# Performance work log

Measured on AMD Instinct MI355X. Metric: run time of the kernel, lower is better.

Reference implementation:

```python
import jax, jax.numpy as jnp
import numpy as np

DIM = 512
HEADS = 16
DIM_HEAD = 64
INNER = HEADS * DIM_HEAD
MAX_T = 32
BASE = 10000.0


def rotate_half(t):
    t1, t2 = jnp.split(t, 2, axis=-1)
    return jnp.concatenate((-t2, t1), axis=-1)


def setup_inputs() -> dict:
    key = jax.random.key(0)
    ks = jax.random.split(key, 12)
    B, T, S = 2, 16, 128
    x = jax.random.normal(ks[0], (B, T, S, DIM), dtype=jnp.float32)
    y = jax.random.normal(ks[1], (B, T, S, DIM), dtype=jnp.float32)
    temporal_mask = jax.random.randint(ks[2], (B, T, T), 0, 2).astype(jnp.int32)
    sc = 1.0 / np.sqrt(DIM)
    Wq = jax.random.normal(ks[3], (DIM, INNER), dtype=jnp.float32) * sc
    Wk = jax.random.normal(ks[4], (DIM, INNER), dtype=jnp.float32) * sc
    Wv = jax.random.normal(ks[5], (DIM, INNER), dtype=jnp.float32) * sc
    Wo = jax.random.normal(ks[6], (INNER, DIM), dtype=jnp.float32) / np.sqrt(INNER)
    bo = jnp.zeros((DIM,), dtype=jnp.float32)
    pos_emb = jax.random.normal(ks[7], (MAX_T, DIM), dtype=jnp.float32)
    gate_w = jax.random.normal(ks[8], (DIM, 1), dtype=jnp.float32) * sc
    gate_b = jnp.zeros((1,), dtype=jnp.float32)
    return {"x": x, "y": y, "temporal_mask": temporal_mask, "Wq": Wq, "Wk": Wk,
            "Wv": Wv, "Wo": Wo, "bo": bo, "pos_emb": pos_emb,
            "gate_w": gate_w, "gate_b": gate_b}


def reference(x, y, temporal_mask, Wq, Wk, Wv, Wo, bo, pos_emb, gate_w, gate_b):
    B, T, S, D = x.shape
    n = T * S
    scale = DIM_HEAD ** (-0.5)
    # temporal positional embedding (T <= MAX_T path)
    tp = pos_emb[:T][None, :, None, :]  # [1,T,1,D]
    x = x + tp
    y = y + tp
    xf = x.reshape(B, n, D)
    yf = y.reshape(B, n, D)
    # NOTE: k is computed from x (as in the source), v from y
    q = (xf @ Wq).reshape(B, n, HEADS, DIM_HEAD).transpose(0, 2, 1, 3)
    k = (xf @ Wk).reshape(B, n, HEADS, DIM_HEAD).transpose(0, 2, 1, 3)
    v = (yf @ Wv).reshape(B, n, HEADS, DIM_HEAD).transpose(0, 2, 1, 3)
    # RoPE over flattened token index
    inv_freq = 1.0 / (BASE ** (jnp.arange(0, DIM_HEAD, 2, dtype=jnp.float32) / DIM_HEAD))
    freqs = jnp.arange(n, dtype=jnp.float32)[:, None] * inv_freq[None, :]  # [n, d/2]
    emb = jnp.concatenate((freqs, freqs), axis=-1)  # [n, d]
    fc = jnp.cos(emb)[None, None, :, :]
    fs = jnp.sin(emb)[None, None, :, :]
    q = q * fc + rotate_half(q) * fs
    k = k * fc + rotate_half(k) * fs
    dots = jnp.einsum('bhid,bhjd->bhij', q, k) * scale  # [B,H,n,n]
    # expand temporal mask [B,T,T] -> [B,1,n,n] block structure
    m = jnp.repeat(jnp.repeat(temporal_mask, S, axis=1), S, axis=2)[:, None, :, :]
    dots = jnp.where(m == 0, -jnp.inf, dots)
    attn = jax.nn.softmax(dots, axis=-1)
    out = jnp.einsum('bhij,bhjd->bhid', attn, v)  # [B,H,n,d]
    out = out.transpose(0, 2, 1, 3).reshape(B, n, INNER)
    out = out @ Wo + bo
    out = out.reshape(B, T, S, D)
    gate = jax.nn.sigmoid(out @ gate_w + gate_b)  # [B,T,S,1]
    return out * gate
```

## Files before the change

### kernel.cpp

```cpp
#include <hip/hip_runtime.h>
#include <hip/hip_bf16.h>

typedef __attribute__((ext_vector_type(4))) short short4v;
typedef __attribute__((ext_vector_type(8))) short short8v;
typedef __attribute__((ext_vector_type(4))) float float4v;
typedef __attribute__((ext_vector_type(2))) unsigned int uint2v;
typedef __attribute__((ext_vector_type(4))) unsigned int uint4v;

#define NTOK 2048
#define MROWS 4096
#define DMODEL 512
#define NINNER 1024
#define DH 64
#define HH 16
#define LOG2E 1.4426950408889634f

__device__ __forceinline__ unsigned short b2s(float f) {
    __hip_bfloat16 h = __float2bfloat16(f);
    return __builtin_bit_cast(unsigned short, h);
}
__device__ __forceinline__ float bf2f(unsigned short h) {
    unsigned int u = ((unsigned int)h) << 16;
    return __builtin_bit_cast(float, u);
}

__device__ __forceinline__ float4v mfma32(short8v a, short8v b, float4v c) {
    return __builtin_amdgcn_mfma_f32_16x16x32_bf16(a, b, c, 0, 0, 0);
}

__device__ __forceinline__ void gld16(const void* g, void* l) {
    __builtin_amdgcn_global_load_lds((const __attribute__((address_space(1))) void*)g,
                                     (__attribute__((address_space(3))) void*)l, 16, 0, 0);
}

__global__ void k_pre(const float* __restrict__ x, const float* __restrict__ y,
                      const float* __restrict__ pe,
                      unsigned short* __restrict__ xpb, unsigned short* __restrict__ ypb,
                      const float* __restrict__ Wq, const float* __restrict__ Wk,
                      const float* __restrict__ Wv, const float* __restrict__ Wo,
                      const float* __restrict__ gwv, const float* __restrict__ gbv,
                      const float* __restrict__ bo,
                      unsigned short* __restrict__ wall, unsigned short* __restrict__ wot,
                      float* __restrict__ ctab, float* __restrict__ stab,
                      unsigned short* __restrict__ gvp, float* __restrict__ bgp) {
    __shared__ float tl[64][65];
    const int blk = blockIdx.x;
    const int tid = threadIdx.x;
    if (blk < 2048) {
        int e0 = (blk * 256 + tid) * 4;
        int row = e0 >> 9, col = e0 & 511;
        int t = (row & (NTOK - 1)) >> 7;
        const float4v xv = *(const float4v*)(x + e0);
        const float4v yv = *(const float4v*)(y + e0);
        const float4v pv = *(const float4v*)(pe + t * DMODEL + col);
        short4v xo, yo;
#pragma unroll
        for (int i = 0; i < 4; ++i) {
            xo[i] = (short)b2s(xv[i] + pv[i]);
            yo[i] = (short)b2s(yv[i] + pv[i]);
        }
        *(short4v*)(xpb + e0) = xo;
        *(short4v*)(ypb + e0) = yo;
    } else if (blk < 2560) {
        int t = blk - 2048;
        const float* W;
        unsigned short* dst;
        int K, N, k0, n0;
        if (t < 384) {
            int which = t / 128, tile = t % 128;
            W = (which == 0) ? Wq : (which == 1) ? Wk : Wv;
            dst = wall + (size_t)which * 1024 * 512;
            K = 512; N = 1024;
            k0 = (tile >> 4) * 64; n0 = (tile & 15) * 64;
        } else {
            int tile = t - 384;
            W = Wo; dst = wot;
            K = 1024; N = 512;
            k0 = (tile >> 3) * 64; n0 = (tile & 7) * 64;
        }
        int tx = tid & 63, ty4 = tid >> 6;
#pragma unroll
        for (int p = 0; p < 16; ++p) {
            int ky = p * 4 + ty4;
            tl[ky][tx] = W[(size_t)(k0 + ky) * N + n0 + tx];
        }
        __syncthreads();
#pragma unroll
        for (int p = 0; p < 16; ++p) {
            int ny = p * 4 + ty4;
            dst[(size_t)(n0 + ny) * K + k0 + tx] = b2s(tl[tx][ny]);
        }
    } else if (blk < 2816) {
        int idx = (blk - 2560) * 256 + tid;
        int p = idx >> 5, j = idx & 31;
        float invf = powf(10000.0f, -(float)(2 * j) * (1.0f / 64.0f));
        float f = (float)p * invf;
        ctab[idx] = cosf(f);
        stab[idx] = sinf(f);
    } else if (blk < 2832) {
        int base = (blk - 2816) * 64;
        int w = tid >> 6, l = tid & 63, l16 = l & 15, g = l >> 4;
        int row = base + w * 16 + l16;
        const float* wr = Wo + (size_t)row * 512 + g * 128;
        const float* gr = gwv + g * 128;
        float s = 0.f;
#pragma unroll
        for (int t = 0; t < 32; ++t) {
            float4v a = *(const float4v*)(wr + t * 4);
            float4v b = *(const float4v*)(gr + t * 4);
            s += a[0] * b[0] + a[1] * b[1] + a[2] * b[2] + a[3] * b[3];
        }
        s += __shfl_xor(s, 16);
        s += __shfl_xor(s, 32);
        if (g == 0) gvp[row] = b2s(s);
    } else {
        if (tid < 64) {
            float s = 0.f;
#pragma unroll
            for (int t = 0; t < 8; ++t) s += bo[tid + t * 64] * gwv[tid + t * 64];
#pragma unroll
            for (int off = 32; off > 0; off >>= 1) s += __shfl_xor(s, off);
            if (tid == 0) bgp[0] = s + gbv[0];
        }
    }
}

__global__ __launch_bounds__(256) void k_qkv(const unsigned short* __restrict__ A,
                                             const unsigned short* __restrict__ A2,
                                             const unsigned short* __restrict__ Bt,
                                             unsigned short* __restrict__ Cq,
                                             unsigned short* __restrict__ Ck,
                                             unsigned short* __restrict__ Cvv,
                                             const float* __restrict__ ctab,
                                             const float* __restrict__ stab,
                                             float scale) {
    __shared__ unsigned short Ab[2][4096];
    __shared__ unsigned short Bb[2][4096];
    const int tid = threadIdx.x;
    const int w = tid >> 6, l = tid & 63, l16 = l & 15, g = l >> 4;
    const int wm = w >> 1, wn = w & 1;
    const int m0 = blockIdx.y * 128, n0 = blockIdx.x * 128;
    const unsigned short* Ap = (n0 >= 2048) ? A2 : A;
    float4v acc[4][4];
#pragma unroll
    for (int i = 0; i < 4; ++i)
#pragma unroll
        for (int j = 0; j < 4; ++j) acc[i][j] = (float4v){0.f, 0.f, 0.f, 0.f};

    auto stage = [&](int t, int buf) {
        int k0 = t * 32;
#pragma unroll
        for (int it = 0; it < 2; ++it) {
            int f = it * 4 + w;
            gld16(Ap + (size_t)(m0 + f * 16 + l16) * 512 + k0 + g * 8, &Ab[buf][f * 512]);
            gld16(Bt + (size_t)(n0 + f * 16 + l16) * 512 + k0 + g * 8, &Bb[buf][f * 512]);
        }
    };

    stage(0, 0);
    __syncthreads();
    for (int t = 0; t < 16; ++t) {
        const int cur = t & 1;
        if (t + 1 < 16) stage(t + 1, cur ^ 1);
        short8v af[4], bf[4];
#pragma unroll
        for (int mi = 0; mi < 4; ++mi)
            af[mi] = *(const short8v*)&Ab[cur][(wm * 4 + mi) * 512 + l * 8];
#pragma unroll
        for (int nj = 0; nj < 4; ++nj)
            bf[nj] = *(const short8v*)&Bb[cur][(wn * 4 + nj) * 512 + l * 8];
        __builtin_amdgcn_s_setprio(1);
#pragma unroll
        for (int mi = 0; mi < 4; ++mi)
#pragma unroll
            for (int nj = 0; nj < 4; ++nj)
                acc[mi][nj] = mfma32(af[mi], bf[nj], acc[mi][nj]);
        __builtin_amdgcn_s_setprio(0);
        __syncthreads();
    }

    const int hh = (n0 + wn * 64) >> 6;
    const int head = hh & 15;
    if (hh < 32) {
        unsigned short* out = (hh < 16) ? Cq : Ck;
        const float sc = (hh < 16) ? scale : 1.0f;
#pragma unroll
        for (int mi = 0; mi < 4; ++mi)
#pragma unroll
            for (int r = 0; r < 4; ++r) {
                int row = m0 + wm * 64 + mi * 16 + g * 4 + r;
                int b = row >> 11, pos = row & (NTOK - 1);
                const float* cr = ctab + pos * 32;
                const float* sr = stab + pos * 32;
                unsigned short* ob = out + (size_t)((b * HH + head) * NTOK + pos) * DH;
#pragma unroll
                for (int nj = 0; nj < 2; ++nj) {
                    int j = nj * 16 + l16;
                    float c = cr[j], s = sr[j];
                    float v1 = acc[mi][nj][r], v2 = acc[mi][nj + 2][r];
                    ob[j] = b2s((v1 * c - v2 * s) * sc);
                    ob[j + 32] = b2s((v2 * c + v1 * s) * sc);
                }
            }
    } else {
#pragma unroll
        for (int mi = 0; mi < 4; ++mi)
#pragma unroll
            for (int nj = 0; nj < 4; ++nj) {
                int d = nj * 16 + l16;
                int row0 = m0 + wm * 64 + mi * 16 + g * 4;
                int b = row0 >> 11, pos0 = row0 & (NTOK - 1);
                short4v o;
#pragma unroll
                for (int r = 0; r < 4; ++r) o[r] = (short)b2s(acc[mi][nj][r]);
                *(short4v*)(Cvv + (size_t)((b * HH + head) * DH + d) * NTOK + pos0) = o;
            }
    }
}

__global__ __launch_bounds__(256) void k_gatev(const unsigned short* __restrict__ otm,
                                               const unsigned short* __restrict__ gv,
                                               const float* __restrict__ bgp,
                                               float* __restrict__ glog) {
    int row = blockIdx.x * 4 + (threadIdx.x >> 6);
    int l = threadIdx.x & 63;
    const unsigned short* pr = otm + (size_t)row * NINNER;
    float acc = 0.f;
#pragma unroll
    for (int c = 0; c < 2; ++c) {
        short8v a = *(const short8v*)(pr + (c * 64 + l) * 8);
        short8v b = *(const short8v*)(gv + (c * 64 + l) * 8);
#pragma unroll
        for (int j = 0; j < 8; ++j)
            acc = fmaf(bf2f((unsigned short)a[j]), bf2f((unsigned short)b[j]), acc);
    }
#pragma unroll
    for (int off = 32; off > 0; off >>= 1) acc += __shfl_xor(acc, off);
    if (l == 0) glog[row] = 1.0f / (1.0f + __expf(-(acc + bgp[0])));
}

__global__ __launch_bounds__(256) void k_oproj(const unsigned short* __restrict__ A,
                                               const unsigned short* __restrict__ Bt,
                                               const float* __restrict__ bo,
                                               const float* __restrict__ glog,
                                               float* __restrict__ out) {
    __shared__ unsigned short Ab[2][4096];
    __shared__ unsigned short Bb[2][2048];
    const int tid = threadIdx.x;
    const int w = tid >> 6, l = tid & 63, l16 = l & 15, g = l >> 4;
    const int m0 = blockIdx.y * 128, n0 = blockIdx.x * 64;
    float4v acc[2][4];
#pragma unroll
    for (int i = 0; i < 2; ++i)
#pragma unroll
        for (int j = 0; j < 4; ++j) acc[i][j] = (float4v){0.f, 0.f, 0.f, 0.f};

    auto stage = [&](int t, int buf) {
        int k0 = t * 32;
#pragma unroll
        for (int s = 0; s < 2; ++s) {
            int fi = s * 4 + w;
            gld16(A + (size_t)(m0 + fi * 16 + l16) * 1024 + k0 + g * 8, &Ab[buf][fi * 512]);
        }
        gld16(Bt + (size_t)(n0 + w * 16 + l16) * 1024 + k0 + g * 8, &Bb[buf][w * 512]);
    };

    stage(0, 0);
    __syncthreads();
    for (int t = 0; t < 32; ++t) {
        const int cur = t & 1;
        if (t + 1 < 32) stage(t + 1, cur ^ 1);
        short8v af[2], bf[4];
#pragma unroll
        for (int mi = 0; mi < 2; ++mi)
            af[mi] = *(const short8v*)&Ab[cur][(w * 2 + mi) * 512 + l * 8];
#pragma unroll
        for (int nj = 0; nj < 4; ++nj)
            bf[nj] = *(const short8v*)&Bb[cur][nj * 512 + l * 8];
        __builtin_amdgcn_s_setprio(1);
#pragma unroll
        for (int mi = 0; mi < 2; ++mi)
#pragma unroll
            for (int nj = 0; nj < 4; ++nj)
                acc[mi][nj] = mfma32(af[mi], bf[nj], acc[mi][nj]);
        __builtin_amdgcn_s_setprio(0);
        __syncthreads();
    }
#pragma unroll
    for (int mi = 0; mi < 2; ++mi) {
        float gl[4];
#pragma unroll
        for (int r = 0; r < 4; ++r)
            gl[r] = glog[m0 + w * 32 + mi * 16 + g * 4 + r];
#pragma unroll
        for (int nj = 0; nj < 4; ++nj) {
            int col = n0 + nj * 16 + l16;
            float bv = bo[col];
#pragma unroll
            for (int r = 0; r < 4; ++r) {
                int row = m0 + w * 32 + mi * 16 + g * 4 + r;
                out[(size_t)row * 512 + col] = (acc[mi][nj][r] + bv) * gl[r];
            }
        }
    }
}

__global__ __launch_bounds__(512) void k_attn(const unsigned short* __restrict__ qh,
                                              const unsigned short* __restrict__ kh,
                                              const unsigned short* __restrict__ vt,
                                              const int* __restrict__ tmask,
                                              unsigned short* __restrict__ otmp) {
    __shared__ unsigned short Kb[3][4096];
    __shared__ unsigned short Vb[2][4096];
    __shared__ int tlist[33];
    const int blk = blockIdx.x;
    const int u = (blk & 7) * 64 + (blk >> 3);
    const int ti = u & 15, h = (u >> 4) & 15, b = u >> 8;
    const int tid = threadIdx.x, w = tid >> 6, l = tid & 63, l16 = l & 15, g = l >> 4;
    if (tid == 0) {
        int c = 0;
        for (int j = 0; j < 16; ++j)
            if (tmask[(b * 16 + ti) * 16 + j]) { tlist[c++] = 2 * j; tlist[c++] = 2 * j + 1; }
        tlist[32] = c;
    }
    __syncthreads();
    const int cnt = tlist[32];
    const unsigned short* qb = qh + (size_t)((b * HH + h) * NTOK) * DH;
    const unsigned short* kb = kh + (size_t)((b * HH + h) * NTOK) * DH;
    const unsigned short* vb = vt + (size_t)((b * HH + h) * DH) * NTOK;
    const int q0 = ti * 128 + w * 16;

    short8v qf[2];
#pragma unroll
    for (int c = 0; c < 2; ++c)
        qf[c] = *(const short8v*)(qb + (size_t)(q0 + l16) * DH + c * 32 + g * 8);

    short8v ones;
#pragma unroll
    for (int j = 0; j < 8; ++j) ones[j] = (short)0x3F80;

    float4v oacc[4];
#pragma unroll
    for (int i = 0; i < 4; ++i) oacc[i] = (float4v){0.f, 0.f, 0.f, 0.f};
    float4v lsum = (float4v){0.f, 0.f, 0.f, 0.f};
    float mx = -1e30f;
    uint4v vrg;
    float4v sA[4], sB[4];

    auto stageK = [&](int st, int buf) {
        const unsigned short* ga =
            kb + (size_t)(st * 64 + (w >> 1) * 16 + l16) * DH + (w & 1) * 32 + g * 8;
        gld16(ga, &Kb[buf][w * 512]);
    };
    auto loadV = [&](int st) {
        const unsigned short* ga =
            vb + (size_t)((w >> 1) * 16 + l16) * NTOK + st * 64 + (w & 1) * 32 + g * 4;
        uint2v lo = *(const uint2v*)ga;
        uint2v hi = *(const uint2v*)(ga + 16);
        vrg = (uint4v){lo[0], lo[1], hi[0], hi[1]};
    };
    auto writeV = [&](int buf) {
        *(uint4v*)&Vb[buf][w * 512 + l * 8] = vrg;
    };
    auto qkcomp = [&](int buf, float4v (&s)[4]) {
#pragma unroll
        for (int jk = 0; jk < 4; ++jk) s[jk] = (float4v){0.f, 0.f, 0.f, 0.f};
        __builtin_amdgcn_s_setprio(1);
#pragma unroll
        for (int jk = 0; jk < 4; ++jk) {
            short8v kf0 = *(const short8v*)&Kb[buf][(jk * 2 + 0) * 512 + l * 8];
            short8v kf1 = *(const short8v*)&Kb[buf][(jk * 2 + 1) * 512 + l * 8];
            s[jk] = mfma32(kf0, qf[0], s[jk]);
            s[jk] = mfma32(kf1, qf[1], s[jk]);
        }
        __builtin_amdgcn_s_setprio(0);
    };

    auto body = [&](int i, float4v (&scur)[4], float4v (&snext)[4]) {
        const bool pre1 = (i + 1 < cnt), pre2 = (i + 2 < cnt);
        if (pre2) stageK(tlist[i + 2], (i + 2) % 3);
        if (pre1) loadV(tlist[i + 1]);
        float tm = -1e30f;
#pragma unroll
        for (int jk = 0; jk < 4; ++jk) {
            float4v s4 = scur[jk];
            tm = fmaxf(tm, fmaxf(fmaxf(s4[0], s4[1]), fmaxf(s4[2], s4[3])));
        }
        tm = fmaxf(tm, __shfl_xor(tm, 16));
        tm = fmaxf(tm, __shfl_xor(tm, 32));
        if (!__all(tm <= mx + 8.0f)) {
            float mnew = fmaxf(mx, tm);
            float alpha = exp2f(mx - mnew);
#pragma unroll
            for (int r = 0; r < 4; ++r) lsum[r] *= alpha;
#pragma unroll
            for (int md = 0; md < 4; ++md)
#pragma unroll
                for (int r = 0; r < 4; ++r) oacc[md][r] *= alpha;
            mx = mnew;
        }
        if (pre1) qkcomp((i + 1) % 3, snext);
        short8v pf[2];
#pragma unroll
        for (int cc = 0; cc < 2; ++cc) {
            short8v pv;
#pragma unroll
            for (int r = 0; r < 4; ++r) {
                pv[r] = (short)b2s(exp2f(scur[2 * cc][r] - mx));
                pv[r + 4] = (short)b2s(exp2f(scur[2 * cc + 1][r] - mx));
            }
            pf[cc] = pv;
        }
        __builtin_amdgcn_s_setprio(1);
#pragma unroll
        for (int cc = 0; cc < 2; ++cc) lsum = mfma32(ones, pf[cc], lsum);
#pragma unroll
        for (int md = 0; md < 4; ++md)
#pragma unroll
            for (int cc = 0; cc < 2; ++cc) {
                short8v vf = *(const short8v*)&Vb[i & 1][(md * 2 + cc) * 512 + l * 8];
                oacc[md] = mfma32(vf, pf[cc], oacc[md]);
            }
        __builtin_amdgcn_s_setprio(0);
        if (pre1) writeV((i + 1) & 1);
        __syncthreads();
    };

    if (cnt > 0) {
        stageK(tlist[0], 0);
        loadV(tlist[0]);
        if (cnt > 1) stageK(tlist[1], 1);
        writeV(0);
        __syncthreads();
        qkcomp(0, sA);
        for (int i = 0; i < cnt; i += 2) {
            body(i, sA, sB);
            if (i + 1 < cnt) body(i + 1, sB, sA);
        }
    }
    float lrow = lsum[0];
    float inv = lrow > 0.f ? 1.0f / lrow : 0.f;
    int q = q0 + l16;
#pragma unroll
    for (int md = 0; md < 4; ++md) {
        short4v o;
#pragma unroll
        for (int r = 0; r < 4; ++r) o[r] = (short)b2s(oacc[md][r] * inv);
        *(short4v*)(otmp + (size_t)(b * NTOK + q) * NINNER + h * DH + md * 16 + g * 4) = o;
    }
}

extern "C" void kernel_launch(void* const* d_in, const int* in_sizes, int n_in,
                              void* d_out, int out_size, void* d_ws, size_t ws_size,
                              hipStream_t stream) {
    (void)in_sizes; (void)n_in; (void)out_size; (void)ws_size;
    const float* x = (const float*)d_in[0];
    const float* y = (const float*)d_in[1];
    const int* tmask = (const int*)d_in[2];
    const float* Wq = (const float*)d_in[3];
    const float* Wk = (const float*)d_in[4];
    const float* Wv = (const float*)d_in[5];
    const float* Wo = (const float*)d_in[6];
    const float* bo = (const float*)d_in[7];
    const float* pe = (const float*)d_in[8];
    const float* gw = (const float*)d_in[9];
    const float* gb = (const float*)d_in[10];

    char* ws = (char*)d_ws;
    const size_t MB = 1u << 20;
    unsigned short* xpb  = (unsigned short*)(ws + 0);
    unsigned short* ypb  = (unsigned short*)(ws + 4 * MB);
    unsigned short* wall = (unsigned short*)(ws + 8 * MB);
    unsigned short* wot  = (unsigned short*)(ws + 11 * MB);
    unsigned short* qh   = (unsigned short*)(ws + 12 * MB);
    unsigned short* kh   = (unsigned short*)(ws + 20 * MB);
    unsigned short* vt   = (unsigned short*)(ws + 28 * MB);
    unsigned short* otm  = (unsigned short*)(ws + 36 * MB);
    float* ct = (float*)(ws + 44 * MB);
    float* st = (float*)(ws + 44 * MB + 256 * 1024);
    unsigned short* gv = (unsigned short*)(ws + 45 * MB);
    float* bg = (float*)(ws + 45 * MB + 4096);
    float* glog = (float*)(ws + 45 * MB + 8192);
    float* outp = (float*)d_out;

    k_pre<<<2833, 256, 0, stream>>>(x, y, pe, xpb, ypb, Wq, Wk, Wv, Wo, gw, gb, bo,
                                    wall, wot, ct, st, gv, bg);
    k_qkv<<<dim3(24, 32), 256, 0, stream>>>(xpb, ypb, wall, qh, kh, vt, ct, st,
                                            0.125f * LOG2E);
    k_attn<<<512, 512, 0, stream>>>(qh, kh, vt, tmask, otm);
    k_gatev<<<1024, 256, 0, stream>>>(otm, gv, bg, glog);
    k_oproj<<<dim3(8, 32), 256, 0, stream>>>(otm, wot, bo, glog, outp);
}
```

Baseline: 123.7 us.

## Deepen K prefetch to four buffers with partial vmcnt waits in attention

The attention kernel now keeps four K stage buffers and prefetches K three tiles ahead instead of two. The full __syncthreads at the end of each step is replaced by an explicit s_waitcnt vmcnt(1) plus a raw barrier, so the newest K load can stay in flight across the barrier. The row max for the next score tile is also computed right after its QK product instead of at the start of the next step. This aims to hide more global-load latency and shorten the critical path, at the cost of more LDS use and reliance on hand-counted vmcnt, which is fragile if the compiler reorders or adds memory operations.

```diff
diff --git a/kernel.cpp b/kernel.cpp
--- a/kernel.cpp
+++ b/kernel.cpp
@@ -310,7 +310,7 @@
                                               const unsigned short* __restrict__ vt,
                                               const int* __restrict__ tmask,
                                               unsigned short* __restrict__ otmp) {
-    __shared__ unsigned short Kb[3][4096];
+    __shared__ unsigned short Kb[4][4096];
     __shared__ unsigned short Vb[2][4096];
     __shared__ int tlist[33];
     const int blk = blockIdx.x;
@@ -346,6 +346,7 @@
     float mx = -1e30f;
     uint4v vrg;
     float4v sA[4], sB[4];
+    float mA = -1e30f, mB = -1e30f;
 
     auto stageK = [&](int st, int buf) {
         const unsigned short* ga =
@@ -375,21 +376,23 @@
         }
         __builtin_amdgcn_s_setprio(0);
     };
-
-    auto body = [&](int i, float4v (&scur)[4], float4v (&snext)[4]) {
-        const bool pre1 = (i + 1 < cnt), pre2 = (i + 2 < cnt);
-        if (pre2) stageK(tlist[i + 2], (i + 2) % 3);
-        if (pre1) loadV(tlist[i + 1]);
-        float tm = -1e30f;
-#pragma unroll
-        for (int jk = 0; jk < 4; ++jk) {
-            float4v s4 = scur[jk];
-            tm = fmaxf(tm, fmaxf(fmaxf(s4[0], s4[1]), fmaxf(s4[2], s4[3])));
-        }
+    auto maxred = [&](const float4v (&s)[4]) -> float {
+        float t0 = fmaxf(fmaxf(s[0][0], s[0][1]), fmaxf(s[0][2], s[0][3]));
+        float t1 = fmaxf(fmaxf(s[1][0], s[1][1]), fmaxf(s[1][2], s[1][3]));
+        float t2 = fmaxf(fmaxf(s[2][0], s[2][1]), fmaxf(s[2][2], s[2][3]));
+        float t3 = fmaxf(fmaxf(s[3][0], s[3][1]), fmaxf(s[3][2], s[3][3]));
+        float tm = fmaxf(fmaxf(t0, t1), fmaxf(t2, t3));
         tm = fmaxf(tm, __shfl_xor(tm, 16));
         tm = fmaxf(tm, __shfl_xor(tm, 32));
-        if (!__all(tm <= mx + 8.0f)) {
-            float mnew = fmaxf(mx, tm);
+        return tm;
+    };
+
+    auto body = [&](int i, float4v (&scur)[4], float& mcur, float4v (&snext)[4], float& mnext) {
+        const bool pre1 = (i + 1 < cnt), pre3 = (i + 3 < cnt);
+        if (pre1) loadV(tlist[i + 1]);
+        if (pre3) stageK(tlist[i + 3], (i + 3) & 3);
+        if (!__all(mcur <= mx + 8.0f)) {
+            float mnew = fmaxf(mx, mcur);
             float alpha = exp2f(mx - mnew);
 #pragma unroll
             for (int r = 0; r < 4; ++r) lsum[r] *= alpha;
@@ -399,7 +402,7 @@
                 for (int r = 0; r < 4; ++r) oacc[md][r] *= alpha;
             mx = mnew;
         }
-        if (pre1) qkcomp((i + 1) % 3, snext);
+        if (pre1) qkcomp((i + 1) & 3, snext);
         short8v pf[2];
 #pragma unroll
         for (int cc = 0; cc < 2; ++cc) {
@@ -422,20 +425,27 @@
                 oacc[md] = mfma32(vf, pf[cc], oacc[md]);
             }
         __builtin_amdgcn_s_setprio(0);
+        if (pre1) mnext = maxred(snext);
         if (pre1) writeV((i + 1) & 1);
-        __syncthreads();
+        if (pre3)
+            asm volatile("s_waitcnt vmcnt(1) lgkmcnt(0)" ::: "memory");
+        else
+            asm volatile("s_waitcnt vmcnt(0) lgkmcnt(0)" ::: "memory");
+        __builtin_amdgcn_s_barrier();
     };
 
     if (cnt > 0) {
+        loadV(tlist[0]);
         stageK(tlist[0], 0);
-        loadV(tlist[0]);
         if (cnt > 1) stageK(tlist[1], 1);
+        if (cnt > 2) stageK(tlist[2], 2);
         writeV(0);
         __syncthreads();
         qkcomp(0, sA);
+        mA = maxred(sA);
         for (int i = 0; i < cnt; i += 2) {
-            body(i, sA, sB);
-            if (i + 1 < cnt) body(i + 1, sB, sA);
+            body(i, sA, mA, sB, mB);
+            if (i + 1 < cnt) body(i + 1, sB, mB, sA, mA);
         }
     }
     float lrow = lsum[0];
```

Result: no change. 125.6 us (+1.6%).
